# Optimization experiments

Measured on AMD Instinct MI355X. Metric: run time of the kernel, lower is better.

## Reference

```python
import jax, jax.numpy as jnp
import numpy as np

N_HEADS = 16
NOPE = 128
ROPE = 64
VDIM = 128
HEAD_DIM = NOPE + ROPE  # 192


def apply_rope(x, cos, sin):
    # x: [B, S, H, D] with D even; pairs (a, b) rotated by complex freqs.
    B, S, H, D = x.shape
    xr = x.reshape(B, S, H, D // 2, 2)
    a, b = xr[..., 0], xr[..., 1]
    c = cos[None, :, None, :]
    s = sin[None, :, None, :]
    out = jnp.stack([a * c - b * s, a * s + b * c], axis=-1)
    return out.reshape(B, S, H, D)


def setup_inputs() -> dict:
    key = jax.random.key(0)
    ks = jax.random.split(key, 8)
    B, S, DIM = 1, 2048, 2048
    x = jax.random.normal(ks[0], (B, S, DIM), dtype=jnp.float32)
    wq = jax.random.normal(ks[1], (N_HEADS * HEAD_DIM, DIM), dtype=jnp.float32) * (DIM ** -0.5)
    wk = jax.random.normal(ks[2], (N_HEADS * HEAD_DIM, DIM), dtype=jnp.float32) * (DIM ** -0.5)
    wv = jax.random.normal(ks[3], (N_HEADS * VDIM, DIM), dtype=jnp.float32) * (DIM ** -0.5)
    wo = jax.random.normal(ks[4], (DIM, N_HEADS * VDIM), dtype=jnp.float32) * ((N_HEADS * VDIM) ** -0.5)
    # rotary freqs: theta = 10000^{-2i/d}, angles = pos * theta
    inv_freq = 1.0 / (10000.0 ** (np.arange(0, ROPE, 2, dtype=np.float32) / ROPE))
    angles = np.arange(S, dtype=np.float32)[:, None] * inv_freq[None, :]  # [S, 32]
    freqs_cos = jnp.asarray(np.cos(angles))
    freqs_sin = jnp.asarray(np.sin(angles))
    # additive causal mask
    mask = jnp.where(jnp.triu(jnp.ones((S, S), dtype=bool), k=1), -1e9, 0.0).astype(jnp.float32)
    return {"x": x, "wq": wq, "wk": wk, "wv": wv, "wo": wo,
            "freqs_cos": freqs_cos, "freqs_sin": freqs_sin, "mask": mask, "start_pos": 0}


def reference(x, wq, wk, wv, wo, freqs_cos, freqs_sin, mask, start_pos):
    B, S, DIM = x.shape
    q = (x @ wq.T).reshape(B, S, N_HEADS, HEAD_DIM)
    k = (x @ wk.T).reshape(B, S, N_HEADS, HEAD_DIM)
    v = (x @ wv.T).reshape(B, S, N_HEADS, VDIM)
    q_nope, q_pe = q[..., :NOPE], q[..., NOPE:]
    k_nope, k_pe = k[..., :NOPE], k[..., NOPE:]
    q_pe = apply_rope(q_pe, freqs_cos, freqs_sin)
    k_pe = apply_rope(k_pe, freqs_cos, freqs_sin)
    scores = (jnp.einsum('bshd,bthd->bsht', q_nope, k_nope)
              + jnp.einsum('bshd,bthd->bsht', q_pe, k_pe)) * (HEAD_DIM ** -0.5)
    scores = scores + mask[None, :, None, :]
    probs = jax.nn.softmax(scores.astype(jnp.float32), axis=-1).astype(x.dtype)
    out = jnp.einsum('bsht,bthd->bshd', probs, v)
    return out.reshape(B, S, N_HEADS * VDIM) @ wo.T
```

## Files before the change

kernel.cpp:

```cpp
#include <hip/hip_runtime.h>
#include <hip/hip_bf16.h>
#include <math.h>

#define NH 16
#define NOPE 128
#define ROPE 64
#define VDIM 128
#define HD 192
#define SEQ 2048
#define DIM 2048
#define QKD (NH * HD)
#define VD  (NH * VDIM)
#define QKVS 8192

typedef __attribute__((ext_vector_type(8))) short short8;
typedef __attribute__((ext_vector_type(4))) short short4v;
typedef __attribute__((ext_vector_type(4))) float f32x4;
typedef unsigned int u32;

#define WAIT_VM8  0x0F78
#define WAIT_VM6  0x0F76
#define WAIT_VM4  0x0F74
#define WAIT_VM3  0x0F73
#define WAIT_VM2  0x0F72
#define WAIT_VM0  0x0F70
#define WAIT_LGKM 0xC07F

static __device__ inline short f2bf(float f) {
  union { float f; unsigned u; } v; v.f = f;
  unsigned r = (v.u + 0x7fffu + ((v.u >> 16) & 1u)) >> 16;
  return (short)r;
}
static __device__ inline u32 packbf(float lo, float hi) {
  return (u32)(unsigned short)f2bf(lo) | ((u32)(unsigned short)f2bf(hi) << 16);
}
static __device__ inline float bf2f(unsigned short u) {
  union { unsigned u; float f; } v; v.u = ((unsigned)u) << 16;
  return v.f;
}

static __device__ __forceinline__ void gload16(const short* g, short* l) {
  __builtin_amdgcn_global_load_lds(
      (const __attribute__((address_space(1))) u32*)g,
      (__attribute__((address_space(3))) u32*)l, 16, 0, 0);
}


#define LSA(pp) (Lsm + (pp) * 65536)
#define LSB(pp) (Lsm + (pp) * 65536 + 32768)

#define RDA(pp, kh, mh) do { \
  const char* p_ = LSA(pp) + abase + (mh) * 8192 + ((kh) ? cx1 : cx0); \
  afr[(mh) * 4 + 0] = *(const short8*)(p_ + 0); \
  afr[(mh) * 4 + 1] = *(const short8*)(p_ + 2048); \
  afr[(mh) * 4 + 2] = *(const short8*)(p_ + 4096); \
  afr[(mh) * 4 + 3] = *(const short8*)(p_ + 6144); \
} while (0)

#define RDB(pp, kh) do { \
  const char* p_ = LSB(pp) + bbase + ((kh) ? cx1 : cx0); \
  bfr[0] = *(const short8*)(p_ + 0); \
  bfr[1] = *(const short8*)(p_ + 2048); \
  bfr[2] = *(const short8*)(p_ + 4096); \
  bfr[3] = *(const short8*)(p_ + 6144); \
} while (0)

#define SGA(kt, c) gload16(srcA[c] + (kt) * 64, (short*)(LSA((kt) & 1) + ((c) * 512 + tid) * 16))
#define SGB(kt, c) gload16(srcB[c] + (kt) * 64, (short*)(LSB((kt) & 1) + ((c) * 512 + tid) * 16))
#define G1S(kt) do { SGA(kt, 0); SGA(kt, 2); SGB(kt, 0); SGB(kt, 1); } while (0)
#define G2S(kt) do { SGA(kt, 1); SGA(kt, 3); SGB(kt, 2); SGB(kt, 3); } while (0)

#define MFMA1(mi, ni) \
  acc[mi][ni] = __builtin_amdgcn_mfma_f32_16x16x32_bf16(afr[mi], bfr[ni], acc[mi][ni], 0, 0, 0)

#define MM(mh) do { \
  MFMA1((mh)*4+0, 0); MFMA1((mh)*4+1, 0); MFMA1((mh)*4+2, 0); MFMA1((mh)*4+3, 0); \
  MFMA1((mh)*4+0, 1); MFMA1((mh)*4+1, 1); MFMA1((mh)*4+2, 1); MFMA1((mh)*4+3, 1); \
  MFMA1((mh)*4+0, 2); MFMA1((mh)*4+1, 2); MFMA1((mh)*4+2, 2); MFMA1((mh)*4+3, 2); \
  MFMA1((mh)*4+0, 3); MFMA1((mh)*4+1, 3); MFMA1((mh)*4+2, 3); MFMA1((mh)*4+3, 3); \
} while (0)

#define GBAR() __builtin_amdgcn_s_barrier()
#define GLGKM0() __builtin_amdgcn_s_waitcnt(WAIT_LGKM)
#define GPRIO1() __builtin_amdgcn_s_setprio(1)
#define GPRIO0() __builtin_amdgcn_s_setprio(0)
#define GNOP ((void)0)

#define TILE(pp, SP1, SP4, VMW) do { \
  RDA(pp, 0, 0); RDB(pp, 0); SP1; \
  GBAR(); GLGKM0(); GPRIO1(); MM(0); GPRIO0(); GBAR(); \
  RDA(pp, 0, 1); \
  GBAR(); GLGKM0(); GPRIO1(); MM(1); GPRIO0(); GBAR(); \
  RDA(pp, 1, 0); RDB(pp, 1); \
  GBAR(); GLGKM0(); GPRIO1(); MM(0); GPRIO0(); GBAR(); \
  RDA(pp, 1, 1); SP4; \
  GBAR(); GLGKM0(); GPRIO1(); MM(1); GPRIO0(); VMW; GBAR(); \
} while (0)

__global__ __launch_bounds__(512, 2) void gemm256_bt(
    const short* __restrict__ A, const short* __restrict__ B,
    short* __restrict__ C, int K, int lda, int ldb, int ldc) {
  __shared__ __align__(16) char Lsm[131072];

  const int tid = threadIdx.x;
  const int lane = tid & 63;
  const int l15 = lane & 15;
  const int quad = lane >> 4;
  const int wv = tid >> 6;
  const int wr = wv >> 2, wc = wv & 3;

  const int bid = blockIdx.x;
  const int xcd = bid & 7;
  const int idx = bid >> 3;
  const int m0 = (idx & 7) * 256;
  const int n0 = (xcd * 4 + (idx >> 3)) * 256;

  const int trow = tid >> 3;
  const int scol = ((tid & 7) * 8) ^ ((trow & 7) * 8);
  const short* srcA[4]; const short* srcB[4];
#pragma unroll
  for (int c = 0; c < 4; ++c) {
    srcA[c] = A + (size_t)(m0 + c * 64 + trow) * lda + scol;
    srcB[c] = B + (size_t)(n0 + c * 64 + trow) * ldb + scol;
  }

  const int abase = (wr * 128 + l15) * 128;
  const int bbase = (wc * 64 + l15) * 128;
  const int cx0 = (quad * 16) ^ ((l15 & 7) * 16);
  const int cx1 = (64 + quad * 16) ^ ((l15 & 7) * 16);

  f32x4 acc[8][4];
#pragma unroll
  for (int i = 0; i < 8; ++i)
#pragma unroll
    for (int j = 0; j < 4; ++j) acc[i][j] = (f32x4)(0.f);
  short8 afr[8], bfr[4];

  const int NT = K >> 6;

  G1S(0); G2S(0); G1S(1);
  __builtin_amdgcn_s_waitcnt(WAIT_VM4);
  GBAR();

  int kt = 0;
  for (; kt + 4 <= NT; kt += 2) {
    TILE(0, G2S(kt + 1), G1S(kt + 2), __builtin_amdgcn_s_waitcnt(WAIT_VM4));
    TILE(1, G2S(kt + 2), G1S(kt + 3), __builtin_amdgcn_s_waitcnt(WAIT_VM4));
  }
  TILE(0, G2S(kt + 1), GNOP, __builtin_amdgcn_s_waitcnt(WAIT_VM0));
  TILE(1, GNOP, GNOP, GNOP);

#pragma unroll
  for (int m = 0; m < 8; ++m) {
    const size_t rb = (size_t)(m0 + wr * 128 + m * 16 + quad * 4) * ldc +
                      n0 + wc * 64 + l15;
#pragma unroll
    for (int n = 0; n < 4; ++n)
#pragma unroll
      for (int r = 0; r < 4; ++r)
        C[rb + (size_t)r * ldc + n * 16] = f2bf(acc[m][n][r]);
  }
}

template <bool BF16OUT>
__global__ __launch_bounds__(256) void gemm_bt(
    const short* __restrict__ A, const short* __restrict__ B,
    void* __restrict__ Cv, int K, int lda, int ldb, int ldc, float oscale) {
  __shared__ __align__(16) short Ls[4][2][4096];

  const int tid = threadIdx.x;
  const int lane = tid & 63;
  const int wave = tid >> 6;
  const int wr = wave >> 1, wc = wave & 1;
  const int lane15 = lane & 15, quad = lane >> 4;
  const int m0 = blockIdx.y * 128, n0 = blockIdx.x * 128;

  const short* gA[4]; const short* gB[4];
#pragma unroll
  for (int i = 0; i < 4; ++i) {
    int gidx = i * 64 + lane;
    int r = gidx >> 2, p = gidx & 3;
    int g = (p ^ ((r >> 1) & 3)) * 8;
    gA[i] = A + (size_t)(m0 + wr * 64 + r) * lda + g;
    gB[i] = B + (size_t)(n0 + wc * 64 + r) * ldb + g;
  }

  f32x4 acc[4][4];
#pragma unroll
  for (int i = 0; i < 4; ++i)
#pragma unroll
    for (int j = 0; j < 4; ++j) acc[i][j] = (f32x4)(0.f);

#pragma unroll
  for (int i = 0; i < 4; ++i) gload16(gA[i], &Ls[wave][0][i * 512]);
#pragma unroll
  for (int i = 0; i < 4; ++i) gload16(gB[i], &Ls[wave][0][2048 + i * 512]);

  const int rsw = (lane15 >> 1) & 3;
  for (int k0 = 0; k0 < K; k0 += 32) {
    const int cur = (k0 >> 5) & 1;
    __builtin_amdgcn_s_waitcnt(WAIT_LGKM);
    if (k0 + 32 < K) {
      const int nxt = cur ^ 1;
#pragma unroll
      for (int i = 0; i < 4; ++i) gload16(gA[i] + k0 + 32, &Ls[wave][nxt][i * 512]);
#pragma unroll
      for (int i = 0; i < 4; ++i) gload16(gB[i] + k0 + 32, &Ls[wave][nxt][2048 + i * 512]);
      __builtin_amdgcn_s_waitcnt(WAIT_VM8);
    } else {
      __builtin_amdgcn_s_waitcnt(WAIT_VM0);
    }
    const short* bufp = &Ls[wave][cur][0];
    short8 af[4], bfv[4];
#pragma unroll
    for (int i = 0; i < 4; ++i)
      af[i] = *(const short8*)&bufp[(i * 16 + lane15) * 32 + (quad ^ rsw) * 8];
#pragma unroll
    for (int j = 0; j < 4; ++j)
      bfv[j] = *(const short8*)&bufp[2048 + (j * 16 + lane15) * 32 + (quad ^ rsw) * 8];
#pragma unroll
    for (int i = 0; i < 4; ++i)
#pragma unroll
      for (int j = 0; j < 4; ++j)
        acc[i][j] = __builtin_amdgcn_mfma_f32_16x16x32_bf16(af[i], bfv[j], acc[i][j], 0, 0, 0);
  }

#pragma unroll
  for (int i = 0; i < 4; ++i)
#pragma unroll
    for (int j = 0; j < 4; ++j)
#pragma unroll
      for (int r = 0; r < 4; ++r) {
        size_t idx = (size_t)(m0 + wr * 64 + i * 16 + quad * 4 + r) * ldc +
                     n0 + wc * 64 + j * 16 + lane15;
        if (BF16OUT)
          ((short*)Cv)[idx] = f2bf(acc[i][j][r] * oscale);
        else
          ((float*)Cv)[idx] = acc[i][j][r];
      }
}

__global__ __launch_bounds__(256) void conv_in(
    const float* __restrict__ x, const float* __restrict__ wq,
    const float* __restrict__ wk, const float* __restrict__ wv,
    short* __restrict__ xb, short* __restrict__ wqkv) {
  const int NX4v = DIM * DIM / 4;
  int i = blockIdx.x * 256 + threadIdx.x;
  float4 f; short* dst; int di;
  if (i < NX4v) {
    f = ((const float4*)x)[i]; dst = xb; di = i;
  } else {
    int j = i - NX4v;
    int row = j >> 9;
    if (row < QKD) f = ((const float4*)wq)[j];
    else if (row < 2 * QKD) f = ((const float4*)wk)[j - QKD * (DIM / 4)];
    else f = ((const float4*)wv)[j - 2 * QKD * (DIM / 4)];
    dst = wqkv; di = j;
  }
  short4v o;
  o.x = f2bf(f.x); o.y = f2bf(f.y); o.z = f2bf(f.z); o.w = f2bf(f.w);
  ((short4v*)dst)[di] = o;
}

#define ROPE_BLKS 4096
#define VT_BLKS   1024
#define WO_BLKS   4096

__global__ __launch_bounds__(256) void post_qkv(
    short* __restrict__ qkv, const float* __restrict__ cosf,
    const float* __restrict__ sinf, short* __restrict__ vtb,
    const float* __restrict__ wo, short* __restrict__ wo_b) {
  __shared__ short tile[64][74];
  const int b = blockIdx.x;
  const int tid = threadIdx.x;

  if (b < ROPE_BLKS) {
    int idx = b * 256 + tid;
    int j = idx & 31;
    int h = (idx >> 5) & (NH - 1);
    int s = idx >> 9;

    float c = cosf[s * 32 + j];
    float sn = sinf[s * 32 + j];
    size_t rowb = (size_t)s * QKVS + h * HD + NOPE + 2 * j;

    u32* pq = (u32*)(qkv + rowb);
    u32 w = *pq;
    float a = bf2f((unsigned short)(w & 0xffff));
    float bb = bf2f((unsigned short)(w >> 16));
    *pq = packbf(a * c - bb * sn, a * sn + bb * c);

    u32* pk = (u32*)(qkv + rowb + QKD);
    w = *pk;
    a = bf2f((unsigned short)(w & 0xffff));
    bb = bf2f((unsigned short)(w >> 16));
    *pk = packbf(a * c - bb * sn, a * sn + bb * c);
  } else if (b < ROPE_BLKS + VT_BLKS) {
    const int bb = b - ROPE_BLKS;
    const int t0 = (bb & 31) * 64;
    const int c0 = (bb >> 5) * 64;
    const short* vb = qkv + 2 * QKD;
#pragma unroll
    for (int i = 0; i < 16; ++i) {
      int idx = i * 256 + tid;
      int r = idx >> 6, c = idx & 63;
      tile[r][c] = vb[(size_t)(t0 + r) * QKVS + c0 + c];
    }
    __syncthreads();
    const int h = c0 >> 7;
    const int dbase = c0 & 127;
#pragma unroll
    for (int i = 0; i < 16; ++i) {
      int idx = i * 256 + tid;
      int d = idx >> 6, t = idx & 63;
      vtb[(size_t)h * VDIM * SEQ + (size_t)(dbase + d) * SEQ + t0 + t] = tile[t][d];
    }
  } else {
    int i = (b - ROPE_BLKS - VT_BLKS) * 256 + tid;
    float4 f = ((const float4*)wo)[i];
    short4v o;
    o.x = f2bf(f.x); o.y = f2bf(f.y); o.z = f2bf(f.z); o.w = f2bf(f.w);
    ((short4v*)wo_b)[i] = o;
  }
}

#define BQ 128
#define BT 64
#define CHT 8
#define MFIX 8.0f

__global__ __launch_bounds__(512, 4) void attn_part(
    const short* __restrict__ qk,
    const short* __restrict__ vtb,
    short* __restrict__ Opart,
    float* __restrict__ lpart)
{
  __shared__ __align__(16) short Ks[2][BT * 192];
  __shared__ __align__(16) short Vt[VDIM * BT];

  const int xcd = blockIdx.x;
  const int i0 = blockIdx.y;
  const int h = xcd + ((i0 >= 40) ? 8 : 0);
  int jj = (i0 >= 40) ? (i0 - 40) : i0;
  int qtb = 15;
  while (jj >= (qtb >> 2) + 1) { jj -= (qtb >> 2) + 1; --qtb; }
  const int chk = jj;

  const int tid = threadIdx.x;
  const int wave = tid >> 6;
  const int lane = tid & 63;
  const int lane15 = lane & 15;
  const int quad = lane >> 4;
  const int g = qtb >> 2;
  const int slot = h * 40 + (g + 1) * (2 * g + (qtb & 3)) + chk;
  const int R0 = qtb * BQ;
  const int NT = 2 * qtb + 2;
  const int kt_beg = chk * CHT;
  const int kt_end = min(kt_beg + CHT, NT);
  const float scale = 0.072168784f;

  const int qrow = R0 + wave * 16 + lane15;
  short8 qf[6];
  const short* qbase = qk + (size_t)qrow * QKVS + h * HD + quad * 8;
#pragma unroll
  for (int kc = 0; kc < 6; ++kc) qf[kc] = *(const short8*)(qbase + kc * 32);
  __builtin_amdgcn_s_waitcnt(WAIT_VM0);
  __builtin_amdgcn_sched_barrier(0);

  const short* kb = qk + QKD;
  int lKoff[3]; const short* gK[3];
#pragma unroll
  for (int i = 0; i < 3; ++i) {
    int id = i * 512 + tid;
    int row = id / 24, cX = id - row * 24;
    int ch = cX ^ (row & 7);
    lKoff[i] = id * 8;
    gK[i] = kb + (size_t)row * QKVS + h * HD + ch * 8;
  }
  const short* gV[2]; short* lV[2];
#pragma unroll
  for (int i = 0; i < 2; ++i) {
    int id = i * 512 + tid;
    int row = id >> 3, cX = id & 7;
    int ch = cX ^ (row & 7);
    lV[i] = &Vt[id * 8];
    gV[i] = vtb + (size_t)h * VDIM * SEQ + (size_t)row * SEQ + ch * 8;
  }

  f32x4 oacc[8];
#pragma unroll
  for (int i = 0; i < 8; ++i) oacc[i] = (f32x4)(0.f);
  float lsum_l = 0.f;

  const int sA = ((lane >> 4) & 1) * 32 + lane15;
  const int sB = sA + 16;
  const bool hiC = (quad >> 1) != 0;

  {
    const size_t t0 = (size_t)kt_beg * BT;
#pragma unroll
    for (int i = 0; i < 3; ++i) gload16(gK[i] + t0 * QKVS, &Ks[0][lKoff[i]]);
#pragma unroll
    for (int i = 0; i < 2; ++i) gload16(gV[i] + t0, lV[i]);
  }
  __builtin_amdgcn_s_waitcnt(WAIT_VM2);
  __builtin_amdgcn_s_barrier();
  __builtin_amdgcn_sched_barrier(0);

  for (int kt = kt_beg; kt < kt_end; ++kt) {
    const int cur = (kt - kt_beg) & 1;
    const bool have = (kt + 1 < kt_end);

    if (have) {
      const size_t tn = (size_t)(kt + 1) * BT;
#pragma unroll
      for (int i = 0; i < 3; ++i) gload16(gK[i] + tn * QKVS, &Ks[cur ^ 1][lKoff[i]]);
    }

    const short* kcur = &Ks[cur][0];
    f32x4 sacc[4];
    __builtin_amdgcn_s_setprio(1);
#pragma unroll
    for (int c = 0; c < 4; ++c) {
      sacc[c] = (f32x4)(0.f);
      const int row = c * 16 + lane15;
#pragma unroll
      for (int kc = 0; kc < 6; ++kc) {
        int cX = (4 * kc + quad) ^ (lane15 & 7);
        short8 kf = *(const short8*)&kcur[row * 192 + cX * 8];
        sacc[c] = __builtin_amdgcn_mfma_f32_16x16x32_bf16(kf, qf[kc], sacc[c], 0, 0, 0);
      }
    }
    __builtin_amdgcn_s_setprio(0);

    if (kt >= 2 * qtb) {
#pragma unroll
      for (int c = 0; c < 4; ++c)
#pragma unroll
        for (int r = 0; r < 4; ++r) {
          int tg = kt * BT + c * 16 + quad * 4 + r;
          int qg = R0 + wave * 16 + lane15;
          if (tg > qg) sacc[c][r] = -1e30f;
        }
    }

#pragma unroll
    for (int c = 0; c < 4; ++c)
#pragma unroll
      for (int r = 0; r < 4; ++r) {
        float p = __expf(sacc[c][r] * scale - MFIX);
        lsum_l += p;
        sacc[c][r] = p;
      }

    u32 w[4][2];
#pragma unroll
    for (int c = 0; c < 4; ++c) {
      w[c][0] = packbf(sacc[c][0], sacc[c][1]);
      w[c][1] = packbf(sacc[c][2], sacc[c][3]);
    }

    union { short8 s; u32 u[4]; } pf0, pf1;
    {
      u32 a0 = __shfl((int)w[0][0], sA), b0 = __shfl((int)w[1][0], sA);
      u32 a1 = __shfl((int)w[0][1], sA), b1 = __shfl((int)w[1][1], sA);
      u32 a2 = __shfl((int)w[0][0], sB), b2 = __shfl((int)w[1][0], sB);
      u32 a3 = __shfl((int)w[0][1], sB), b3 = __shfl((int)w[1][1], sB);
      pf0.u[0] = hiC ? b0 : a0; pf0.u[1] = hiC ? b1 : a1;
      pf0.u[2] = hiC ? b2 : a2; pf0.u[3] = hiC ? b3 : a3;
      u32 c0 = __shfl((int)w[2][0], sA), d0 = __shfl((int)w[3][0], sA);
      u32 c1 = __shfl((int)w[2][1], sA), d1 = __shfl((int)w[3][1], sA);
      u32 c2 = __shfl((int)w[2][0], sB), d2 = __shfl((int)w[3][0], sB);
      u32 c3 = __shfl((int)w[2][1], sB), d3 = __shfl((int)w[3][1], sB);
      pf1.u[0] = hiC ? d0 : c0; pf1.u[1] = hiC ? d1 : c1;
      pf1.u[2] = hiC ? d2 : c2; pf1.u[3] = hiC ? d3 : c3;
    }

    if (have) __builtin_amdgcn_s_waitcnt(WAIT_VM3);
    else      __builtin_amdgcn_s_waitcnt(WAIT_VM0);
    __builtin_amdgcn_s_barrier();
    __builtin_amdgcn_sched_barrier(0);

    __builtin_amdgcn_s_setprio(1);
#pragma unroll
    for (int ch = 0; ch < 8; ++ch) {
      const int row = ch * 16 + lane15;
      int cX0 = quad ^ (lane15 & 7);
      int cX1 = (4 + quad) ^ (lane15 & 7);
      short8 vf0 = *(const short8*)&Vt[row * 64 + cX0 * 8];
      short8 vf1 = *(const short8*)&Vt[row * 64 + cX1 * 8];
      oacc[ch] = __builtin_amdgcn_mfma_f32_16x16x32_bf16(pf0.s, vf0, oacc[ch], 0, 0, 0);
      oacc[ch] = __builtin_amdgcn_mfma_f32_16x16x32_bf16(pf1.s, vf1, oacc[ch], 0, 0, 0);
    }
    __builtin_amdgcn_s_setprio(0);

    if (have) {
      __builtin_amdgcn_s_waitcnt(WAIT_LGKM);
      __builtin_amdgcn_s_barrier();
      const size_t tn = (size_t)(kt + 1) * BT;
#pragma unroll
      for (int i = 0; i < 2; ++i) gload16(gV[i] + tn, lV[i]);
      __builtin_amdgcn_s_waitcnt(WAIT_VM2);
      __builtin_amdgcn_s_barrier();
      __builtin_amdgcn_sched_barrier(0);
    }
  }

  short* op = Opart + (size_t)slot * (128 * 128);
#pragma unroll
  for (int ch = 0; ch < 8; ++ch)
#pragma unroll
    for (int r = 0; r < 4; ++r)
      op[(wave * 16 + quad * 4 + r) * 128 + ch * 16 + lane15] = f2bf(oacc[ch][r]);

  float s = lsum_l;
  s += __shfl_xor(s, 16, 64);
  s += __shfl_xor(s, 32, 64);
  if (quad == 0)
    lpart[(size_t)slot * 128 + wave * 16 + lane15] = s;
}

__global__ __launch_bounds__(256) void attn_combine(
    const short* __restrict__ Opart, const float* __restrict__ lpart,
    short* __restrict__ aob) {
  const int qt64 = blockIdx.x, h = blockIdx.y;
  const int qtb = qt64 >> 1;
  const int half = qt64 & 1;
  const int g = qtb >> 2;
  const int nact = g + 1;
  const int base = h * 40 + (g + 1) * (2 * g + (qtb & 3));
  const int tid = threadIdx.x;
  const int row = tid >> 2;
  const int cg = (tid & 3) * 32;

  float acc[32];
#pragma unroll
  for (int e = 0; e < 32; ++e) acc[e] = 0.f;
  float lsum = 0.f;

  for (int c = 0; c < nact; ++c) {
    const short* sp = Opart + (size_t)(base + c) * (128 * 128) +
                      (half * 64 + row) * 128 + cg;
    lsum += lpart[(size_t)(base + c) * 128 + half * 64 + row];
#pragma unroll
    for (int gg = 0; gg < 4; ++gg) {
      short8 vv = *(const short8*)(sp + gg * 8);
#pragma unroll
      for (int e = 0; e < 8; ++e) acc[gg * 8 + e] += bf2f((unsigned short)vv[e]);
    }
  }

  float inv = 1.f / lsum;
#pragma unroll
  for (int gg = 0; gg < 4; ++gg) {
    short8 ov;
#pragma unroll
    for (int e = 0; e < 8; ++e) ov[e] = f2bf(acc[gg * 8 + e] * inv);
    *(short8*)(aob + (size_t)(qt64 * 64 + row) * VD + h * 128 + cg + gg * 8) = ov;
  }
}

extern "C" void kernel_launch(void* const* d_in, const int* in_sizes, int n_in,
                              void* d_out, int out_size, void* d_ws, size_t ws_size,
                              hipStream_t stream) {
  const float* x  = (const float*)d_in[0];
  const float* wq = (const float*)d_in[1];
  const float* wk = (const float*)d_in[2];
  const float* wv = (const float*)d_in[3];
  const float* wo = (const float*)d_in[4];
  const float* fc = (const float*)d_in[5];
  const float* fs = (const float*)d_in[6];

  char* ws8 = (char*)d_ws;
  short* xb    = (short*)(ws8 + 0);
  short* wo_b  = (short*)(ws8 + 0);
  short* wqkv  = (short*)(ws8 + 8388608);
  short* vtb   = (short*)(ws8 + 8388608);
  short* Opart = (short*)(ws8 + 16777216);
  float* lpart = (float*)(ws8 + 37748736);
  short* qkv   = (short*)(ws8 + 41943040);
  short* aob   = qkv;
  float* out   = (float*)d_out;

  const int NX4 = DIM * DIM / 4;
  const int NQKV4 = QKVS * DIM / 4;

  conv_in<<<(NX4 + NQKV4) / 256, 256, 0, stream>>>(x, wq, wk, wv, xb, wqkv);

  gemm256_bt<<<dim3((QKVS / 256) * (SEQ / 256)), 512, 0, stream>>>(
      xb, wqkv, qkv, DIM, DIM, DIM, QKVS);

  post_qkv<<<ROPE_BLKS + VT_BLKS + WO_BLKS, 256, 0, stream>>>(
      qkv, fc, fs, vtb, wo, wo_b);

  attn_part<<<dim3(8, 80), 512, 0, stream>>>(qkv, vtb, Opart, lpart);
  attn_combine<<<dim3(SEQ / 64, NH), 256, 0, stream>>>(Opart, lpart, aob);

  gemm_bt<false><<<dim3(DIM / 128, SEQ / 128), 256, 0, stream>>>(
      aob, wo_b, out, DIM, VD, DIM, DIM, 1.0f);
}
```

Baseline: 300.8 us.

## Share LDS tiles across waves in output GEMM with XCD-aware block mapping

The output-projection GEMM no longer has each wave stage its own private A/B slices in LDS. All 256 threads now cooperatively load a shared 128x64 K-tile, synchronised with block barriers, and the K step grows from 32 to 64. Blocks are remapped to a 1D grid so that blocks landing on the same XCD cover neighbouring M/N tiles, which should improve L2 reuse. It also adds launch_bounds occupancy 2 and setprio around the MFMA bursts, at the cost of two barriers per K iteration.

```diff
diff --git a/kernel.cpp b/kernel.cpp
--- a/kernel.cpp
+++ b/kernel.cpp
@@ -163,26 +163,31 @@
 }
 
 template <bool BF16OUT>
-__global__ __launch_bounds__(256) void gemm_bt(
+__global__ __launch_bounds__(256, 2) void gemm128_bt(
     const short* __restrict__ A, const short* __restrict__ B,
     void* __restrict__ Cv, int K, int lda, int ldb, int ldc, float oscale) {
-  __shared__ __align__(16) short Ls[4][2][4096];
+  __shared__ __align__(16) short Ls[2][2][8192];
 
   const int tid = threadIdx.x;
   const int lane = tid & 63;
+  const int l15 = lane & 15;
+  const int quad = lane >> 4;
   const int wave = tid >> 6;
   const int wr = wave >> 1, wc = wave & 1;
-  const int lane15 = lane & 15, quad = lane >> 4;
-  const int m0 = blockIdx.y * 128, n0 = blockIdx.x * 128;
-
-  const short* gA[4]; const short* gB[4];
-#pragma unroll
-  for (int i = 0; i < 4; ++i) {
-    int gidx = i * 64 + lane;
-    int r = gidx >> 2, p = gidx & 3;
-    int g = (p ^ ((r >> 1) & 3)) * 8;
-    gA[i] = A + (size_t)(m0 + wr * 64 + r) * lda + g;
-    gB[i] = B + (size_t)(n0 + wc * 64 + r) * ldb + g;
+
+  const int bid = blockIdx.x;
+  const int xcd = bid & 7;
+  const int ii = bid >> 3;
+  const int m0 = (((xcd & 3) << 2) + (ii & 3)) * 128;
+  const int n0 = (((xcd >> 2) << 3) + (ii >> 2)) * 128;
+
+  const int trow = tid >> 3;
+  const int scol = (((tid & 7) ^ (trow & 7))) * 8;
+  const short* srcA[4]; const short* srcB[4];
+#pragma unroll
+  for (int c = 0; c < 4; ++c) {
+    srcA[c] = A + (size_t)(m0 + c * 32 + trow) * lda + scol;
+    srcB[c] = B + (size_t)(n0 + c * 32 + trow) * ldb + scol;
   }
 
   f32x4 acc[4][4];
@@ -191,38 +196,56 @@
 #pragma unroll
     for (int j = 0; j < 4; ++j) acc[i][j] = (f32x4)(0.f);
 
-#pragma unroll
-  for (int i = 0; i < 4; ++i) gload16(gA[i], &Ls[wave][0][i * 512]);
-#pragma unroll
-  for (int i = 0; i < 4; ++i) gload16(gB[i], &Ls[wave][0][2048 + i * 512]);
-
-  const int rsw = (lane15 >> 1) & 3;
-  for (int k0 = 0; k0 < K; k0 += 32) {
-    const int cur = (k0 >> 5) & 1;
-    __builtin_amdgcn_s_waitcnt(WAIT_LGKM);
-    if (k0 + 32 < K) {
-      const int nxt = cur ^ 1;
-#pragma unroll
-      for (int i = 0; i < 4; ++i) gload16(gA[i] + k0 + 32, &Ls[wave][nxt][i * 512]);
-#pragma unroll
-      for (int i = 0; i < 4; ++i) gload16(gB[i] + k0 + 32, &Ls[wave][nxt][2048 + i * 512]);
+  const int NT = K >> 6;
+
+#pragma unroll
+  for (int c = 0; c < 4; ++c) gload16(srcA[c], &Ls[0][0][(c * 256 + tid) * 8]);
+#pragma unroll
+  for (int c = 0; c < 4; ++c) gload16(srcB[c], &Ls[0][1][(c * 256 + tid) * 8]);
+
+  for (int kt = 0; kt < NT; ++kt) {
+    const int cur = kt & 1;
+    if (kt + 1 < NT) {
+      const int kc = (kt + 1) * 64;
+#pragma unroll
+      for (int c = 0; c < 4; ++c)
+        gload16(srcA[c] + kc, &Ls[cur ^ 1][0][(c * 256 + tid) * 8]);
+#pragma unroll
+      for (int c = 0; c < 4; ++c)
+        gload16(srcB[c] + kc, &Ls[cur ^ 1][1][(c * 256 + tid) * 8]);
       __builtin_amdgcn_s_waitcnt(WAIT_VM8);
     } else {
       __builtin_amdgcn_s_waitcnt(WAIT_VM0);
     }
-    const short* bufp = &Ls[wave][cur][0];
-    short8 af[4], bfv[4];
-#pragma unroll
-    for (int i = 0; i < 4; ++i)
-      af[i] = *(const short8*)&bufp[(i * 16 + lane15) * 32 + (quad ^ rsw) * 8];
-#pragma unroll
-    for (int j = 0; j < 4; ++j)
-      bfv[j] = *(const short8*)&bufp[2048 + (j * 16 + lane15) * 32 + (quad ^ rsw) * 8];
-#pragma unroll
-    for (int i = 0; i < 4; ++i)
-#pragma unroll
-      for (int j = 0; j < 4; ++j)
-        acc[i][j] = __builtin_amdgcn_mfma_f32_16x16x32_bf16(af[i], bfv[j], acc[i][j], 0, 0, 0);
+    __builtin_amdgcn_s_barrier();
+
+    const short* la = &Ls[cur][0][0];
+    const short* lb = &Ls[cur][1][0];
+#pragma unroll
+    for (int kh = 0; kh < 2; ++kh) {
+      short8 af[4], bfv[4];
+#pragma unroll
+      for (int m = 0; m < 4; ++m) {
+        int row = wr * 64 + m * 16 + l15;
+        int ch = (kh * 4 + quad) ^ (l15 & 7);
+        af[m] = *(const short8*)&la[row * 64 + ch * 8];
+      }
+#pragma unroll
+      for (int n = 0; n < 4; ++n) {
+        int row = wc * 64 + n * 16 + l15;
+        int ch = (kh * 4 + quad) ^ (l15 & 7);
+        bfv[n] = *(const short8*)&lb[row * 64 + ch * 8];
+      }
+      __builtin_amdgcn_s_setprio(1);
+#pragma unroll
+      for (int m = 0; m < 4; ++m)
+#pragma unroll
+        for (int n = 0; n < 4; ++n)
+          acc[m][n] = __builtin_amdgcn_mfma_f32_16x16x32_bf16(af[m], bfv[n], acc[m][n], 0, 0, 0);
+      __builtin_amdgcn_s_setprio(0);
+    }
+    __builtin_amdgcn_s_waitcnt(WAIT_LGKM);
+    __builtin_amdgcn_s_barrier();
   }
 
 #pragma unroll
@@ -232,7 +255,7 @@
 #pragma unroll
       for (int r = 0; r < 4; ++r) {
         size_t idx = (size_t)(m0 + wr * 64 + i * 16 + quad * 4 + r) * ldc +
-                     n0 + wc * 64 + j * 16 + lane15;
+                     n0 + wc * 64 + j * 16 + l15;
         if (BF16OUT)
           ((short*)Cv)[idx] = f2bf(acc[i][j][r] * oscale);
         else
@@ -596,6 +619,6 @@
   attn_part<<<dim3(8, 80), 512, 0, stream>>>(qkv, vtb, Opart, lpart);
   attn_combine<<<dim3(SEQ / 64, NH), 256, 0, stream>>>(Opart, lpart, aob);
 
-  gemm_bt<false><<<dim3(DIM / 128, SEQ / 128), 256, 0, stream>>>(
+  gemm128_bt<false><<<dim3(256), 256, 0, stream>>>(
       aob, wo_b, out, DIM, VD, DIM, DIM, 1.0f);
 }
```

Result: no change. 296.6 us (-1.4%).
